# Performance work log

Measured on AMD Instinct MI355X. Metric: run time of the kernel, lower is better.

## Reference

```python
import jax, jax.numpy as jnp
import numpy as np
import math

D_MODEL = 512
NUM_HEADS = 8
B, L = 2, 4096
EPS_NORM = 1e-8
PLASTICITY = 1.0


def setup_inputs() -> dict:
    key = jax.random.key(0)
    ks = jax.random.split(key, 6)
    D, H = D_MODEL, NUM_HEADS
    std = 1.0 / math.sqrt(D)
    x = jax.random.normal(ks[0], (B, L, D), dtype=jnp.float32)
    qkv_w = jax.random.normal(ks[1], (3 * D, D), dtype=jnp.float32) * std
    qkv_b = jnp.zeros((3 * D,), dtype=jnp.float32)
    out_w = jax.random.normal(ks[2], (D, D), dtype=jnp.float32) * std
    out_b = jnp.zeros((D,), dtype=jnp.float32)
    decay_w = jax.random.normal(ks[3], (H, D), dtype=jnp.float32) * 0.02
    decay_b = jnp.full((H,), 4.0, dtype=jnp.float32)
    norm_scale = jnp.ones((D,), dtype=jnp.float32)
    return {"x": x, "qkv_w": qkv_w, "qkv_b": qkv_b, "out_w": out_w,
            "out_b": out_b, "decay_w": decay_w, "decay_b": decay_b,
            "norm_scale": norm_scale}


def _hebbian_forward(x, qkv_w, qkv_b, out_w, out_b, decay_w, decay_b, norm_scale):
    Bsz, Lsz, D = x.shape
    H = NUM_HEADS
    E = D // H
    # QKV projection (torch Linear: y = x @ W.T + b)
    qkv = x @ qkv_w.T + qkv_b
    q, k, v = jnp.split(qkv, 3, axis=-1)
    q = q.reshape(Bsz, Lsz, H, E)
    k = k.reshape(Bsz, Lsz, H, E)
    v = v.reshape(Bsz, Lsz, H, E)
    # feature map: elu(x) + 1
    q = (jax.nn.elu(q) + 1.0) / math.sqrt(E)
    k = jax.nn.elu(k) + 1.0
    # input-dependent decay per head
    decay_logits = x @ decay_w.T + decay_b          # (B,L,H)
    lambdas = (0.9 + 0.1 * jax.nn.sigmoid(decay_logits)) * PLASTICITY
    log_lambdas = jnp.log(jnp.clip(lambdas, 1e-6))[..., None]   # (B,L,H,1)
    log_lambda_cum = jnp.clip(jnp.cumsum(log_lambdas, axis=1), -50.0, 50.0)
    decay_k = jnp.exp(-log_lambda_cum)
    decay_q = jnp.exp(log_lambda_cum)
    k_decayed = k * decay_k
    q_decayed = q * decay_q
    # outer-product memory state cumsum: (B,L,H,E,E)
    kv = jnp.einsum('blhe,blhf->blhef', k_decayed, v)
    memory_state = jnp.cumsum(kv, axis=1)
    k_sum_decayed = jnp.cumsum(k_decayed, axis=1)
    num = jnp.einsum('blhe,blhef->blhf', q_decayed, memory_state)
    den = jnp.einsum('blhe,blhe->blh', q_decayed, k_sum_decayed)[..., None] + 1e-6
    out = (num / den).reshape(Bsz, Lsz, D)
    out = out @ out_w.T + out_b
    # RMSNorm (dropout is identity in eval)
    rnorm = jax.lax.rsqrt(jnp.mean(out * out, axis=-1, keepdims=True) + EPS_NORM)
    return out * rnorm * norm_scale


def reference(x, qkv_w, qkv_b, out_w, out_b, decay_w, decay_b, norm_scale):
    return _hebbian_forward(x, qkv_w, qkv_b, out_w, out_b, decay_w, decay_b, norm_scale)
```

## Files before the change

### kernel.cpp

```cpp
#include <hip/hip_runtime.h>

typedef unsigned short u16;
typedef unsigned int u32;

#define B_ 2
#define L_ 4096
#define D_ 512
#define H_ 8
#define E_ 64
#define M_ (B_*L_)
#define TD (3*D_)
#define NCH (L_/64)
#define BH (B_*H_)

typedef short bf16x8 __attribute__((ext_vector_type(8)));
typedef float f32x4 __attribute__((ext_vector_type(4)));

__device__ __forceinline__ float bf2f(u16 u){ return __uint_as_float(((u32)u)<<16); }
__device__ __forceinline__ u16 f2bf(float f){
  u32 u = __float_as_uint(f);
  u32 r = u + 0x7FFFu + ((u>>16)&1u);
  return (u16)(r>>16);
}
__device__ __forceinline__ float elu1(float v){ return v>0.f ? v+1.f : __expf(v); }

__device__ __forceinline__ void async_ld16(const u16* g, u16* l){
  __builtin_amdgcn_global_load_lds(
      (const __attribute__((address_space(1))) void*)g,
      (__attribute__((address_space(3))) void*)l, 16, 0, 0);
}

__global__ __launch_bounds__(256) void decay_conv_kernel(const float* __restrict__ x,
    const float* __restrict__ dw, const float* __restrict__ db,
    const float* __restrict__ qw, const float* __restrict__ ow,
    float* __restrict__ ll, u16* __restrict__ xb,
    u16* __restrict__ qwb, u16* __restrict__ owb)
{
  int blk = blockIdx.x;
  if (blk < 2048){
    int wv = threadIdx.x>>6, lane = threadIdx.x&63;
    int m = blk*4 + wv;
    float xr[8];
    #pragma unroll
    for (int i=0;i<8;i++) xr[i] = x[(size_t)m*D_ + lane + 64*i];
    #pragma unroll
    for (int i=0;i<8;i++) xb[(size_t)m*D_ + lane + 64*i] = f2bf(xr[i]);
    int b = m >> 12, l = m & (L_-1);
    float acc8[8];
    #pragma unroll
    for (int h=0; h<8; h++){
      float a = 0.f;
      #pragma unroll
      for (int i=0;i<8;i++) a += xr[i]*dw[h*D_ + lane + 64*i];
      acc8[h] = a;
    }
    float s4[4];
    #pragma unroll
    for (int i=0;i<4;i++){
      float a = acc8[2*i], bb = acc8[2*i+1];
      bool odd = lane & 1;
      float keep = odd ? bb : a;
      float send = odd ? a : bb;
      s4[i] = keep + __shfl_xor(send, 1);
    }
    float s2[2];
    #pragma unroll
    for (int j=0;j<2;j++){
      float a = s4[2*j], bb = s4[2*j+1];
      bool sel = (lane>>1) & 1;
      float keep = sel ? bb : a;
      float send = sel ? a : bb;
      s2[j] = keep + __shfl_xor(send, 2);
    }
    float r;
    {
      bool sel = (lane>>2) & 1;
      float keep = sel ? s2[1] : s2[0];
      float send = sel ? s2[0] : s2[1];
      r = keep + __shfl_xor(send, 4);
    }
    r += __shfl_xor(r, 8);
    r += __shfl_xor(r, 16);
    r += __shfl_xor(r, 32);
    if (lane < 8){
      float z = r + db[lane];
      float lam = 0.9f + 0.1f/(1.f + __expf(-z));
      ll[((b*H_+lane)*L_) + l] = __logf(lam);
    }
  } else {
    int gid = (blk-2048)*256 + threadIdx.x;
    const float* src; u16* dst; int off;
    if (gid < 196608){ src = qw; dst = qwb; off = gid; }
    else { src = ow; dst = owb; off = gid - 196608; }
    float4 v = ((const float4*)src)[off];
    ushort4 o; o.x=f2bf(v.x); o.y=f2bf(v.y); o.z=f2bf(v.z); o.w=f2bf(v.w);
    ((ushort4*)dst)[off] = o;
  }
}

__global__ __launch_bounds__(256) void scan_kernel(const float* __restrict__ ll,
    float* __restrict__ cb)
{
  int bh = blockIdx.x, t = threadIdx.x;
  int lane = t & 63, wv = t >> 6;
  const float* p = ll + (size_t)bh*L_ + t*16;
  float s[16];
  #pragma unroll
  for (int q=0;q<4;q++){
    float4 v = *(const float4*)(p + q*4);
    s[q*4+0]=v.x; s[q*4+1]=v.y; s[q*4+2]=v.z; s[q*4+3]=v.w;
  }
  #pragma unroll
  for (int i=1;i<16;i++) s[i] += s[i-1];
  float tot = s[15];
  float ws = tot;
  #pragma unroll
  for (int off=1; off<64; off<<=1){
    float tmp = __shfl_up(ws, off);
    if (lane >= off) ws += tmp;
  }
  __shared__ float wsum[4];
  if (lane == 63) wsum[wv] = ws;
  __syncthreads();
  float base = 0.f;
  #pragma unroll
  for (int w2=0; w2<3; w2++) if (w2 < wv) base += wsum[w2];
  float ex = base + ws - tot;
  float* c = cb + (size_t)bh*L_ + t*16;
  #pragma unroll
  for (int i=0;i<16;i++) c[i] = fminf(50.f, fmaxf(-50.f, ex + s[i]));
}

__global__ __launch_bounds__(256) void gemm_qkv_fused(const u16* __restrict__ A,
    const u16* __restrict__ W, const float* __restrict__ bias,
    const float* __restrict__ cb,
    u16* __restrict__ qc, u16* __restrict__ kc, u16* __restrict__ vc)
{
  __shared__ u16 SM[24576];
  const int K = 512;
  int n0 = blockIdx.x*128, m0 = blockIdx.y*128;
  int t = threadIdx.x, wave = t>>6, lane = t&63;
  int wm = (wave>>1)*64, wn = (wave&1)*64;
  f32x4 acc[4][4] = {};
  int srow = wave*32 + (lane>>2);
  int scol = (lane&3)*8;
  const u16* gA = A + (size_t)(m0+srow)*K + scol;
  const u16* gB = W + (size_t)(n0+srow)*K + scol;
  int q8 = (lane>>4)*8, r16 = lane&15;
  auto STAGE = [&](u16* buf, int k0){
    u16* lA = buf + wave*1024;
    u16* lB = buf + 4096 + wave*1024;
    async_ld16(gA + k0,                lA);
    async_ld16(gA + k0 + 16*(size_t)K, lA + 512);
    async_ld16(gB + k0,                lB);
    async_ld16(gB + k0 + 16*(size_t)K, lB + 512);
  };
  u16 *cB = SM, *nB = SM + 8192, *tB = SM + 16384;
  STAGE(cB, 0);
  STAGE(nB, 32);
  for (int k0=0; k0<K; k0+=32){
    if (k0 + 32 < K) asm volatile("s_waitcnt vmcnt(4)" ::: "memory");
    else             asm volatile("s_waitcnt vmcnt(0)" ::: "memory");
    __builtin_amdgcn_s_barrier();
    if (k0 + 64 < K) STAGE(tB, k0 + 64);
    bf16x8 af[4], bfr[4];
    #pragma unroll
    for (int i=0;i<4;i++) af[i]  = *(const bf16x8*)&cB[(wm + i*16 + r16)*32 + q8];
    #pragma unroll
    for (int j=0;j<4;j++) bfr[j] = *(const bf16x8*)&cB[4096 + (wn + j*16 + r16)*32 + q8];
    #pragma unroll
    for (int i=0;i<4;i++)
      #pragma unroll
      for (int j=0;j<4;j++)
        acc[i][j] = __builtin_amdgcn_mfma_f32_16x16x32_bf16(af[i], bfr[j], acc[i][j], 0,0,0);
    u16* tmp = cB; cB = nB; nB = tB; tB = tmp;
  }
  __syncthreads();
  int g = lane>>4;
  #pragma unroll
  for (int j=0;j<4;j++){
    int col = wn + j*16 + r16;
    float bv = bias[n0 + col];
    #pragma unroll
    for (int i=0;i<4;i++){
      int rbase = wm + i*16 + g*4;
      #pragma unroll
      for (int r=0;r<4;r++)
        SM[(rbase+r)*136 + col] = f2bf(acc[i][j][r] + bv);
    }
  }
  __syncthreads();
  int sec = n0 >> 9;
  #pragma unroll
  for (int u=0;u<8;u++){
    int idx = t + 256*u;
    int rloc = idx >> 4;
    int colg = (idx & 15) * 8;
    int row = m0 + rloc;
    int nn = (n0 + colg) & 511;
    int h2 = nn>>6, e0 = nn&63;
    int bh2 = ((row>>12)<<3) | h2;
    int bid = (bh2<<6) | ((row>>6)&63);
    int l6 = row & 63;
    union { uint4 v; u16 s[8]; } dat;
    dat.v = *(const uint4*)&SM[rloc*136 + colg];
    size_t a = ((size_t)(bid*2 + (e0>>5)))*2048 + (size_t)l6*32 + (e0&31);
    if (sec == 0){
      float eqc = __expf(cb[((size_t)bh2<<12) | (row & 4095)])*0.125f;
      #pragma unroll
      for (int jj=0;jj<8;jj++) dat.s[jj] = f2bf(elu1(bf2f(dat.s[jj]))*eqc);
      *(uint4*)(qc + a) = dat.v;
    } else if (sec == 1){
      float ekc = __expf(-cb[((size_t)bh2<<12) | (row & 4095)]);
      #pragma unroll
      for (int jj=0;jj<8;jj++) dat.s[jj] = f2bf(elu1(bf2f(dat.s[jj]))*ekc);
      *(uint4*)(kc + a) = dat.v;
    } else {
      *(uint4*)(vc + a) = dat.v;
    }
  }
}

__global__ __launch_bounds__(256) void chunk_sums_kernel(const u16* __restrict__ kc,
    const u16* __restrict__ vc, u16* __restrict__ Stc, float* __restrict__ ksc)
{
  int bid = blockIdx.x;
  __shared__ u16 Kc[4096], Vc[4096];
  __shared__ u16 Ktl[5120], Vtl[5120];
  __shared__ float ksr[256];
  int t = threadIdx.x, w = t>>6, lane = t&63;
  {
    const u16* gk = kc + (size_t)bid*4096 + w*1024 + lane*8;
    const u16* gv = vc + (size_t)bid*4096 + w*1024 + lane*8;
    async_ld16(gk,       Kc + w*1024);
    async_ld16(gk + 512, Kc + w*1024 + 512);
    async_ld16(gv,       Vc + w*1024);
    async_ld16(gv + 512, Vc + w*1024 + 512);
  }
  __syncthreads();
  int e = t & 63, jq = t >> 6;
  {
    u16 kv[16] __attribute__((aligned(16)));
    u16 vv[16] __attribute__((aligned(16)));
    float ksum = 0.f;
    #pragma unroll
    for (int jj=0;jj<16;jj++){
      int j = jq*16+jj;
      kv[jj] = Kc[(e>>5)*2048 + j*32 + (e&31)];
      ksum += bf2f(kv[jj]);
      vv[jj] = Vc[(e>>5)*2048 + j*32 + (e&31)];
    }
    int kh2 = jq>>1, jl = (jq&1)*16;
    u16* kt = &Ktl[(kh2*64 + e)*40 + jl];
    u16* vt = &Vtl[(kh2*64 + e)*40 + jl];
    *(uint4*)kt     = *(const uint4*)&kv[0];
    *(uint4*)(kt+8) = *(const uint4*)&kv[8];
    *(uint4*)vt     = *(const uint4*)&vv[0];
    *(uint4*)(vt+8) = *(const uint4*)&vv[8];
    ksr[t] = ksum;
  }
  __syncthreads();
  int r16 = lane & 15, q8 = (lane>>4)*8;
  bf16x8 av[2];
  #pragma unroll
  for (int kh=0;kh<2;kh++)
    av[kh] = *(const bf16x8*)&Vtl[(kh*64 + w*16 + r16)*40 + q8];
  f32x4 acc[4] = {};
  #pragma unroll
  for (int et=0;et<4;et++)
    #pragma unroll
    for (int kh=0;kh<2;kh++){
      bf16x8 bv = *(const bf16x8*)&Ktl[(kh*64 + et*16 + r16)*40 + q8];
      acc[et] = __builtin_amdgcn_mfma_f32_16x16x32_bf16(av[kh], bv, acc[et], 0,0,0);
    }
  #pragma unroll
  for (int et=0;et<4;et++){
    int eh = et>>1, el = (et&1)*16 + r16;
    #pragma unroll
    for (int r=0;r<4;r++){
      int f = w*16 + (lane>>4)*4 + r;
      Stc[((size_t)bid*2 + eh)*2048 + f*32 + el] = f2bf(acc[et][r]);
    }
  }
  if (t < 64) ksc[bid*64 + t] = ksr[t] + ksr[64+t] + ksr[128+t] + ksr[192+t];
}

__global__ __launch_bounds__(256) void chunk_prefix_kernel(u16* __restrict__ Stc,
    float* __restrict__ ksc)
{
  int blk = blockIdx.x, t = threadIdx.x;
  if (blk < 128){
    int gid = blk*256 + t;
    int bh = gid >> 11, e2 = gid & 2047;
    u32* p = (u32*)Stc + (size_t)bh*131072 + e2;
    float r0 = 0.f, r1 = 0.f;
    #pragma unroll 16
    for (int ch=0; ch<NCH; ch++){
      u32 v = p[ch*2048];
      float lo = bf2f((u16)(v & 0xffffu));
      float hi = bf2f((u16)(v >> 16));
      p[ch*2048] = (u32)f2bf(r0) | ((u32)f2bf(r1) << 16);
      r0 += lo; r1 += hi;
    }
  } else {
    int gid2 = (blk-128)*256 + t;
    int bh2 = gid2 >> 6, e = gid2 & 63;
    float* kp = ksc + bh2*4096 + e;
    float kr = 0.f;
    #pragma unroll 8
    for (int ch=0; ch<NCH; ch++){
      float v = kp[ch*64]; kp[ch*64] = kr; kr += v;
    }
  }
}

__global__ __launch_bounds__(256) void chunk_out_kernel(const u16* __restrict__ qc,
    const u16* __restrict__ kc, const u16* __restrict__ vc,
    const u16* __restrict__ Stc, const float* __restrict__ ksc,
    u16* __restrict__ attn)
{
  int bid = blockIdx.x;
  int bh = bid >> 6, ch = bid & 63;
  int b = bh >> 3, h = bh & 7;
  __shared__ u16 Kb_l[4096];
  __shared__ u16 Vc_l[4096];
  __shared__ u16 St_l[4096];
  __shared__ u16 Vt[5120];
  __shared__ u16 Ab[4096];
  __shared__ float R2[320];
  int t = threadIdx.x, w = t>>6, lane = t&63;
  size_t mbase = (size_t)b*L_ + ch*64;
  {
    const u16* gk = kc  + (size_t)bid*4096 + w*1024 + lane*8;
    const u16* gv = vc  + (size_t)bid*4096 + w*1024 + lane*8;
    const u16* gs = Stc + (size_t)bid*4096 + w*1024 + lane*8;
    async_ld16(gk,       Kb_l + w*1024);
    async_ld16(gk + 512, Kb_l + w*1024 + 512);
    async_ld16(gv,       Vc_l + w*1024);
    async_ld16(gv + 512, Vc_l + w*1024 + 512);
    async_ld16(gs,       St_l + w*1024);
    async_ld16(gs + 512, St_l + w*1024 + 512);
  }
  int r16 = lane & 15, q8 = (lane>>4)*8;
  const u16* qg = qc + (size_t)bid*4096;
  bf16x8 aq[2];
  #pragma unroll
  for (int eh=0;eh<2;eh++)
    aq[eh] = *(const bf16x8*)(qg + eh*2048 + (w*16 + r16)*32 + q8);
  int l4 = t>>2, q4 = t&3;
  int ehd = q4>>1, el0 = (q4&1)*16;
  bf16x8 x1 = *(const bf16x8*)(qg + ehd*2048 + l4*32 + el0);
  bf16x8 x2 = *(const bf16x8*)(qg + ehd*2048 + l4*32 + el0 + 8);
  union { float4 v[4]; float f[16]; } kp;
  #pragma unroll
  for (int qq=0;qq<4;qq++)
    kp.v[qq] = *(const float4*)(ksc + bid*64 + q4*16 + qq*4);
  __syncthreads();
  {
    int e = t & 63, jq = t >> 6;
    u16 vv[16] __attribute__((aligned(16)));
    #pragma unroll
    for (int jj=0;jj<16;jj++)
      vv[jj] = Vc_l[(e>>5)*2048 + (jq*16+jj)*32 + (e&31)];
    int jh = jq>>1, jl = (jq&1)*16;
    u16* vt = &Vt[(jh*64 + e)*40 + jl];
    *(uint4*)vt     = *(const uint4*)&vv[0];
    *(uint4*)(vt+8) = *(const uint4*)&vv[8];
  }
  f32x4 accA[4] = {};
  #pragma unroll
  for (int jt=0;jt<4;jt++)
    #pragma unroll
    for (int eh=0;eh<2;eh++){
      bf16x8 bv = *(const bf16x8*)&Kb_l[(eh*64 + jt*16 + r16)*32 + q8];
      accA[jt] = __builtin_amdgcn_mfma_f32_16x16x32_bf16(aq[eh], bv, accA[jt], 0,0,0);
    }
  float dkp = 0.f;
  #pragma unroll
  for (int i=0;i<8;i++)
    dkp += bf2f((u16)x1[i])*kp.f[i] + bf2f((u16)x2[i])*kp.f[8+i];
  #pragma unroll
  for (int jt=0;jt<4;jt++)
    #pragma unroll
    for (int r=0;r<4;r++){
      int lr = w*16 + ((lane>>4)<<2) + r;
      int j  = jt*16 + r16;
      Ab[((jt>>1)*64 + lr)*32 + (jt&1)*16 + r16] = (j <= lr) ? f2bf(accA[jt][r]) : (u16)0;
    }
  __syncthreads();
  float dA = 0.f;
  {
    int jh2 = q4>>1, jl0 = (q4&1)*16;
    bf16x8 y1 = *(const bf16x8*)&Ab[(jh2*64 + l4)*32 + jl0];
    bf16x8 y2 = *(const bf16x8*)&Ab[(jh2*64 + l4)*32 + jl0 + 8];
    #pragma unroll
    for (int i=0;i<8;i++) dA += bf2f((u16)y1[i]) + bf2f((u16)y2[i]);
  }
  R2[t] = dkp + dA;
  __syncthreads();
  if (t < 64) R2[256+t] = R2[t*4] + R2[t*4+1] + R2[t*4+2] + R2[t*4+3] + 1e-6f;
  bf16x8 aA[2];
  #pragma unroll
  for (int jh=0;jh<2;jh++)
    aA[jh] = *(const bf16x8*)&Ab[(jh*64 + w*16 + r16)*32 + q8];
  f32x4 acc[4] = {};
  #pragma unroll
  for (int ft=0;ft<4;ft++){
    #pragma unroll
    for (int jh=0;jh<2;jh++){
      bf16x8 bv = *(const bf16x8*)&Vt[(jh*64 + ft*16 + r16)*40 + q8];
      acc[ft] = __builtin_amdgcn_mfma_f32_16x16x32_bf16(aA[jh], bv, acc[ft], 0,0,0);
    }
    #pragma unroll
    for (int eh=0;eh<2;eh++){
      bf16x8 bv = *(const bf16x8*)&St_l[(eh*64 + ft*16 + r16)*32 + q8];
      acc[ft] = __builtin_amdgcn_mfma_f32_16x16x32_bf16(aq[eh], bv, acc[ft], 0,0,0);
    }
  }
  __syncthreads();
  float inv[4];
  #pragma unroll
  for (int r=0;r<4;r++) inv[r] = 1.f / R2[256 + w*16 + ((lane>>4)<<2) + r];
  #pragma unroll
  for (int ft=0;ft<4;ft++)
    #pragma unroll
    for (int r=0;r<4;r++){
      int lr = w*16 + ((lane>>4)<<2) + r;
      attn[(mbase + lr)*D_ + h*64 + ft*16 + r16] = f2bf(acc[ft][r]*inv[r]);
    }
}

__global__ __launch_bounds__(256) void gemm_rms_kernel(const u16* __restrict__ A,
    const u16* __restrict__ W, const float* __restrict__ bias,
    const float* __restrict__ gnorm, float* __restrict__ out)
{
  __shared__ u16 As[2][1024];
  __shared__ u16 Bs[2][16384];
  __shared__ float ssq_l[4][32];
  __shared__ float rinv_l[32];
  int m0 = blockIdx.x*32;
  int t = threadIdx.x, wave = t>>6, lane = t&63;
  int wn = wave*128;
  int r16 = lane&15, q8 = (lane>>4)*8;
  f32x4 acc[2][8] = {};
  int scol = (t&3)*8;
  const u16* gB = W + (size_t)(t>>2)*512 + scol;
  const u16* gA = A + (size_t)(m0 + (t>>2))*512 + scol;
  {
    if (wave < 2) async_ld16(gA, As[0] + wave*512);
    #pragma unroll
    for (int it=0; it<8; it++)
      async_ld16(gB + it*32768, Bs[0] + wave*512 + it*2048);
  }
  int cur = 0;
  for (int k0=0; k0<512; k0+=32){
    asm volatile("s_waitcnt vmcnt(0)" ::: "memory");
    __builtin_amdgcn_s_barrier();
    if (k0 < 480){
      if (wave < 2) async_ld16(gA + k0+32, As[cur^1] + wave*512);
      #pragma unroll
      for (int it=0; it<8; it++)
        async_ld16(gB + k0+32 + it*32768, Bs[cur^1] + wave*512 + it*2048);
    }
    bf16x8 af0 = *(const bf16x8*)&As[cur][r16*32 + q8];
    bf16x8 af1 = *(const bf16x8*)&As[cur][(16 + r16)*32 + q8];
    #pragma unroll
    for (int j=0;j<8;j++){
      bf16x8 bv = *(const bf16x8*)&Bs[cur][(wn + j*16 + r16)*32 + q8];
      acc[0][j] = __builtin_amdgcn_mfma_f32_16x16x32_bf16(af0, bv, acc[0][j], 0,0,0);
      acc[1][j] = __builtin_amdgcn_mfma_f32_16x16x32_bf16(af1, bv, acc[1][j], 0,0,0);
    }
    cur ^= 1;
  }
  int g = lane>>4;
  float bv8[8], gv8[8];
  #pragma unroll
  for (int j=0;j<8;j++){ int col = wn + j*16 + r16; bv8[j] = bias[col]; gv8[j] = gnorm[col]; }
  float ssq[2][4] = {};
  #pragma unroll
  for (int i=0;i<2;i++)
    #pragma unroll
    for (int j=0;j<8;j++)
      #pragma unroll
      for (int r=0;r<4;r++){
        float v = acc[i][j][r] + bv8[j];
        acc[i][j][r] = v;
        ssq[i][r] += v*v;
      }
  #pragma unroll
  for (int off=1; off<16; off<<=1)
    #pragma unroll
    for (int i=0;i<2;i++)
      #pragma unroll
      for (int r=0;r<4;r++)
        ssq[i][r] += __shfl_xor(ssq[i][r], off);
  if (r16 == 0){
    #pragma unroll
    for (int i=0;i<2;i++)
      #pragma unroll
      for (int r=0;r<4;r++)
        ssq_l[wave][i*16 + g*4 + r] = ssq[i][r];
  }
  __syncthreads();
  if (t < 32)
    rinv_l[t] = rsqrtf((ssq_l[0][t]+ssq_l[1][t]+ssq_l[2][t]+ssq_l[3][t])*(1.f/512.f) + 1e-8f);
  __syncthreads();
  #pragma unroll
  for (int i=0;i<2;i++)
    #pragma unroll
    for (int r=0;r<4;r++){
      int row = m0 + i*16 + g*4 + r;
      float ri = rinv_l[i*16 + g*4 + r];
      #pragma unroll
      for (int j=0;j<8;j++)
        out[(size_t)row*512 + wn + j*16 + r16] = acc[i][j][r]*ri*gv8[j];
    }
}

extern "C" void kernel_launch(void* const* d_in, const int* in_sizes, int n_in,
                              void* d_out, int out_size, void* d_ws, size_t ws_size,
                              hipStream_t stream)
{
  const float* x     = (const float*)d_in[0];
  const float* w_qkv = (const float*)d_in[1];
  const float* b_qkv = (const float*)d_in[2];
  const float* w_out = (const float*)d_in[3];
  const float* b_out = (const float*)d_in[4];
  const float* w_dec = (const float*)d_in[5];
  const float* b_dec = (const float*)d_in[6];
  const float* gnorm = (const float*)d_in[7];
  float* out = (float*)d_out;

  char* ws = (char*)d_ws;
  u16*   qc   = (u16*)(ws);
  u16*   kc   = (u16*)(ws + 8388608);
  u16*   vc   = (u16*)(ws + 16777216);
  u16*   Stc  = (u16*)(ws + 25165824);
  float* ksc  = (float*)(ws + 33554432);
  float* ll   = (float*)(ws + 33816576);
  float* cb   = (float*)(ws + 34078720);
  u16*   xb   = (u16*)(ws + 34340864);
  u16*   qwb  = (u16*)(ws + 42729472);
  u16*   owb  = (u16*)(ws + 44302336);
  u16*   attn = xb;

  decay_conv_kernel<<<dim3(3072), dim3(256), 0, stream>>>(x, w_dec, b_dec, w_qkv, w_out,
                                                          ll, xb, qwb, owb);
  scan_kernel<<<dim3(BH), dim3(256), 0, stream>>>(ll, cb);
  gemm_qkv_fused<<<dim3(TD/128, M_/128), dim3(256), 0, stream>>>(xb, qwb, b_qkv, cb, qc, kc, vc);
  chunk_sums_kernel<<<dim3(BH*NCH), dim3(256), 0, stream>>>(kc, vc, Stc, ksc);
  chunk_prefix_kernel<<<dim3(132), dim3(256), 0, stream>>>(Stc, ksc);
  chunk_out_kernel<<<dim3(BH*NCH), dim3(256), 0, stream>>>(qc, kc, vc, Stc, ksc, attn);
  gemm_rms_kernel<<<dim3(M_/32), dim3(256), 0, stream>>>(attn, owb, b_out, gnorm, out);
}
```

Baseline: 152.5 us.

## Remap block indices for XCD-local L2 reuse and load state directly into registers

Block IDs in the conversion, QKV GEMM and chunk kernels are remapped so that blocks landing on the same XCD (round-robin by blockIdx mod 8) work on contiguous row ranges and chunks. This is meant to make data written by one kernel more likely to be read from the same XCD's L2 by the next. Separately, chunk_out now loads the prefix-state matrix straight from global memory into MFMA B-operand registers instead of staging it through LDS. That drops one shared buffer and its barrier dependency, at the cost of more registers and uncoalesced fragment loads.

Measured after the change: 150.7 us. About the same (-1.2%).

```diff
diff --git a/kernel.cpp b/kernel.cpp
--- a/kernel.cpp
+++ b/kernel.cpp
@@ -39,7 +39,7 @@
   int blk = blockIdx.x;
   if (blk < 2048){
     int wv = threadIdx.x>>6, lane = threadIdx.x&63;
-    int m = blk*4 + wv;
+    int m = ((blk&7)<<10) + ((blk>>3)<<2) + wv;
     float xr[8];
     #pragma unroll
     for (int i=0;i<8;i++) xr[i] = x[(size_t)m*D_ + lane + 64*i];
@@ -138,7 +138,11 @@
 {
   __shared__ u16 SM[24576];
   const int K = 512;
-  int n0 = blockIdx.x*128, m0 = blockIdx.y*128;
+  int bid0 = blockIdx.x;
+  int xcd = bid0 & 7, idx = bid0 >> 3;
+  int mblk = xcd*8 + idx/12;
+  int nblk = idx % 12;
+  int n0 = nblk*128, m0 = mblk*128;
   int t = threadIdx.x, wave = t>>6, lane = t&63;
   int wm = (wave>>1)*64, wn = (wave&1)*64;
   f32x4 acc[4][4] = {};
@@ -193,9 +197,9 @@
   int sec = n0 >> 9;
   #pragma unroll
   for (int u=0;u<8;u++){
-    int idx = t + 256*u;
-    int rloc = idx >> 4;
-    int colg = (idx & 15) * 8;
+    int idx2 = t + 256*u;
+    int rloc = idx2 >> 4;
+    int colg = (idx2 & 15) * 8;
     int row = m0 + rloc;
     int nn = (n0 + colg) & 511;
     int h2 = nn>>6, e0 = nn&63;
@@ -221,10 +225,19 @@
   }
 }
 
+__device__ __forceinline__ int chunk_bid_remap(int i){
+  int xcd = i & 7;
+  int b = xcd >> 2, chhi = xcd & 3;
+  int idx = i >> 3;
+  int h = idx >> 4, chlo = idx & 15;
+  int ch = (chhi<<4) | chlo;
+  return (((b<<3)|h)<<6) | ch;
+}
+
 __global__ __launch_bounds__(256) void chunk_sums_kernel(const u16* __restrict__ kc,
     const u16* __restrict__ vc, u16* __restrict__ Stc, float* __restrict__ ksc)
 {
-  int bid = blockIdx.x;
+  int bid = chunk_bid_remap(blockIdx.x);
   __shared__ u16 Kc[4096], Vc[4096];
   __shared__ u16 Ktl[5120], Vtl[5120];
   __shared__ float ksr[256];
@@ -319,12 +332,11 @@
     const u16* __restrict__ Stc, const float* __restrict__ ksc,
     u16* __restrict__ attn)
 {
-  int bid = blockIdx.x;
+  int bid = chunk_bid_remap(blockIdx.x);
   int bh = bid >> 6, ch = bid & 63;
   int b = bh >> 3, h = bh & 7;
   __shared__ u16 Kb_l[4096];
   __shared__ u16 Vc_l[4096];
-  __shared__ u16 St_l[4096];
   __shared__ u16 Vt[5120];
   __shared__ u16 Ab[4096];
   __shared__ float R2[320];
@@ -333,20 +345,22 @@
   {
     const u16* gk = kc  + (size_t)bid*4096 + w*1024 + lane*8;
     const u16* gv = vc  + (size_t)bid*4096 + w*1024 + lane*8;
-    const u16* gs = Stc + (size_t)bid*4096 + w*1024 + lane*8;
     async_ld16(gk,       Kb_l + w*1024);
     async_ld16(gk + 512, Kb_l + w*1024 + 512);
     async_ld16(gv,       Vc_l + w*1024);
     async_ld16(gv + 512, Vc_l + w*1024 + 512);
-    async_ld16(gs,       St_l + w*1024);
-    async_ld16(gs + 512, St_l + w*1024 + 512);
   }
   int r16 = lane & 15, q8 = (lane>>4)*8;
-  const u16* qg = qc + (size_t)bid*4096;
-  bf16x8 aq[2];
-  #pragma unroll
-  for (int eh=0;eh<2;eh++)
+  const u16* qg = qc  + (size_t)bid*4096;
+  const u16* sg = Stc + (size_t)bid*4096;
+  bf16x8 aq[2], sfr[2][4];
+  #pragma unroll
+  for (int eh=0;eh<2;eh++){
     aq[eh] = *(const bf16x8*)(qg + eh*2048 + (w*16 + r16)*32 + q8);
+    #pragma unroll
+    for (int ft=0;ft<4;ft++)
+      sfr[eh][ft] = *(const bf16x8*)(sg + (eh*64 + ft*16 + r16)*32 + q8);
+  }
   int l4 = t>>2, q4 = t&3;
   int ehd = q4>>1, el0 = (q4&1)*16;
   bf16x8 x1 = *(const bf16x8*)(qg + ehd*2048 + l4*32 + el0);
@@ -412,10 +426,8 @@
       acc[ft] = __builtin_amdgcn_mfma_f32_16x16x32_bf16(aA[jh], bv, acc[ft], 0,0,0);
     }
     #pragma unroll
-    for (int eh=0;eh<2;eh++){
-      bf16x8 bv = *(const bf16x8*)&St_l[(eh*64 + ft*16 + r16)*32 + q8];
-      acc[ft] = __builtin_amdgcn_mfma_f32_16x16x32_bf16(aq[eh], bv, acc[ft], 0,0,0);
-    }
+    for (int eh=0;eh<2;eh++)
+      acc[ft] = __builtin_amdgcn_mfma_f32_16x16x32_bf16(aq[eh], sfr[eh][ft], acc[ft], 0,0,0);
   }
   __syncthreads();
   float inv[4];
@@ -547,7 +559,7 @@
   decay_conv_kernel<<<dim3(3072), dim3(256), 0, stream>>>(x, w_dec, b_dec, w_qkv, w_out,
                                                           ll, xb, qwb, owb);
   scan_kernel<<<dim3(BH), dim3(256), 0, stream>>>(ll, cb);
-  gemm_qkv_fused<<<dim3(TD/128, M_/128), dim3(256), 0, stream>>>(xb, qwb, b_qkv, cb, qc, kc, vc);
+  gemm_qkv_fused<<<dim3(768), dim3(256), 0, stream>>>(xb, qwb, b_qkv, cb, qc, kc, vc);
   chunk_sums_kernel<<<dim3(BH*NCH), dim3(256), 0, stream>>>(kc, vc, Stc, ksc);
   chunk_prefix_kernel<<<dim3(132), dim3(256), 0, stream>>>(Stc, ksc);
   chunk_out_kernel<<<dim3(BH*NCH), dim3(256), 0, stream>>>(qc, kc, vc, Stc, ksc, attn);
```
